# Performance work log

Hardware: AMD Instinct MI355X
Metric: run time of the kernel (lower is better)

## Reference

```python
import jax, jax.numpy as jnp
import numpy as np
from jax import lax

N, T, F_IN = 2048, 32, 5      # stocks, lookback, OHLCV features
H, L, R = 64, 2, 8            # lstm hidden, lstm layers, relation types
GAT_H = 16                    # GAT3 hard-coded hidden width
EDGE_P = 0.05                 # relation-mask edge density
NEG = -1e9


def setup_inputs() -> dict:
    key = jax.random.key(0)
    ks = jax.random.split(key, 20)
    f32 = jnp.float32

    def nrm(k, shape, s=0.1):
        return jax.random.normal(k, shape, f32) * s

    inp = {}
    inp["inputs"] = jax.random.normal(ks[0], (N, T, F_IN), f32)
    inp["relation"] = jax.random.normal(ks[1], (N, N, R), f32)
    mask = jax.random.uniform(ks[2], (N, N)) < EDGE_P
    inp["rel_mask"] = jnp.where(mask, 0.0, NEG).astype(f32)
    # rel_weight: Linear(R, 1)
    inp["rel_w_W"] = nrm(ks[3], (1, R))
    inp["rel_w_b"] = jnp.zeros((1,), f32)
    # 2-layer LSTM (PyTorch layout: w_ih [4H, in], w_hh [4H, H], gate order i,f,g,o)
    inp["w_ih0"] = nrm(ks[4], (4 * H, F_IN)); inp["w_hh0"] = nrm(ks[5], (4 * H, H))
    inp["b_ih0"] = jnp.zeros((4 * H,), f32);  inp["b_hh0"] = jnp.zeros((4 * H,), f32)
    inp["w_ih1"] = nrm(ks[6], (4 * H, H));    inp["w_hh1"] = nrm(ks[7], (4 * H, H))
    inp["b_ih1"] = jnp.zeros((4 * H,), f32);  inp["b_hh1"] = jnp.zeros((4 * H,), f32)
    # GATConv1: hidden -> 16, heads=1 ; GATConv2: 16 -> hidden, heads=1 (lin has no bias in PyG)
    inp["gat1_W"]  = nrm(ks[8], (H, GAT_H));  inp["gat1_as"] = nrm(ks[9], (GAT_H,))
    inp["gat1_ad"] = nrm(ks[10], (GAT_H,));   inp["gat1_b"]  = jnp.zeros((GAT_H,), f32)
    inp["gat2_W"]  = nrm(ks[11], (GAT_H, H)); inp["gat2_as"] = nrm(ks[12], (H,))
    inp["gat2_ad"] = nrm(ks[13], (H,));       inp["gat2_b"]  = jnp.zeros((H,), f32)
    # fc: hidden -> 1
    inp["fc_W"] = nrm(ks[14], (H, 1)); inp["fc_b"] = jnp.zeros((1,), f32)
    return inp


def _lstm_layer(x, w_ih, w_hh, b_ih, b_hh):
    # x: [N, T, in] -> [N, T, H]; PyTorch LSTM equations, zero initial state.
    n = x.shape[0]
    h0 = jnp.zeros((n, w_hh.shape[1]), x.dtype)

    def step(carry, xt):
        h, c = carry
        g = xt @ w_ih.T + h @ w_hh.T + (b_ih + b_hh)   # [N, 4H]
        i, f, gg, o = jnp.split(g, 4, axis=-1)
        c = jax.nn.sigmoid(f) * c + jax.nn.sigmoid(i) * jnp.tanh(gg)
        h = jax.nn.sigmoid(o) * jnp.tanh(c)
        return (h, c), h

    _, hs = lax.scan(step, (h0, h0), jnp.swapaxes(x, 0, 1))  # scan over T
    return jnp.swapaxes(hs, 0, 1)


def _gat(h_in, adj, W, a_s, a_d, b):
    # Dense single-head GATConv over a boolean adjacency adj[src, dst].
    h = h_in @ W                                    # [N, out]
    e = jax.nn.leaky_relu((h @ a_s)[:, None] + (h @ a_d)[None, :], 0.2)  # [src, dst]
    e = jnp.where(adj, e, NEG)
    alpha = jax.nn.softmax(e, axis=0)               # softmax over sources per target
    return alpha.T @ h + b                          # aggregate into targets


def _forward(inputs, relation, rel_mask, rel_w_W, rel_w_b,
             w_ih0, w_hh0, b_ih0, b_hh0, w_ih1, w_hh1, b_ih1, b_hh1,
             gat1_W, gat1_as, gat1_ad, gat1_b,
             gat2_W, gat2_as, gat2_ad, gat2_b, fc_W, fc_b):
    x = _lstm_layer(inputs, w_ih0, w_hh0, b_ih0, b_hh0)
    x = _lstm_layer(x, w_ih1, w_hh1, b_ih1, b_hh1)
    x = x[:, -1, :]                                       # [N, H] last timestep
    rel_w = jnp.einsum('nmr,r->nm', relation, rel_w_W[0]) + rel_w_b[0]  # Linear(R,1)[...,-1]
    inner = x @ x.T                                       # [N, N] similarity
    weight = inner @ rel_w                                # [N, N]
    ws = jax.nn.softmax(rel_mask + weight, axis=1)        # masked entries underflow to 0
    adj = ws > 0                                          # == nonzero edge extraction
    idx = jnp.arange(adj.shape[0])
    adj = adj.at[idx, idx].set(True)                      # GATConv add_self_loops
    h = jax.nn.relu(_gat(x, adj, gat1_W, gat1_as, gat1_ad, gat1_b))
    out = _gat(h, adj, gat2_W, gat2_as, gat2_ad, gat2_b)
    return jax.nn.leaky_relu(out @ fc_W + fc_b, 0.2)      # [N, 1] prediction


def reference(inputs, relation, rel_mask, rel_w_W, rel_w_b,
              w_ih0, w_hh0, b_ih0, b_hh0, w_ih1, w_hh1, b_ih1, b_hh1,
              gat1_W, gat1_as, gat1_ad, gat1_b,
              gat2_W, gat2_as, gat2_ad, gat2_b, fc_W, fc_b):
    return _forward(inputs, relation, rel_mask, rel_w_W, rel_w_b,
                    w_ih0, w_hh0, b_ih0, b_hh0, w_ih1, w_hh1, b_ih1, b_hh1,
                    gat1_W, gat1_as, gat1_ad, gat1_b,
                    gat2_W, gat2_as, gat2_ad, gat2_b, fc_W, fc_b)
```

## Files before the change

### kernel.cpp

```cpp
#include <hip/hip_runtime.h>
#include <math.h>

#define NN 2048
#define TT 32
#define FIN 5
#define HH 64
#define G4 256
#define GATH 16
#define CAP 256

__device__ __forceinline__ float sigf(float x) {
    return 1.0f / (1.0f + __expf(-x));
}
__device__ __forceinline__ float tanh_fast(float x) {
    x = fminf(fmaxf(x, -15.0f), 15.0f);
    float t = __expf(2.0f * x);
    return (t - 1.0f) / (t + 1.0f);
}
__device__ __forceinline__ float dot4(float4 a, float4 b) {
    return a.x * b.x + a.y * b.y + a.z * b.z + a.w * b.w;
}
__device__ __forceinline__ float lrelu_exp(float x) {
    x = (x > 0.0f) ? x : 0.2f * x;
    return __expf(x);
}

#define LNB 2
__global__ __launch_bounds__(256, 1)
void k_lstm(
    const float* __restrict__ inputs,
    const float* __restrict__ w_ih0, const float* __restrict__ w_hh0,
    const float* __restrict__ b_ih0, const float* __restrict__ b_hh0,
    const float* __restrict__ w_ih1, const float* __restrict__ w_hh1,
    const float* __restrict__ b_ih1, const float* __restrict__ b_hh1,
    float* __restrict__ x_out)
{
    __shared__ float x_lds[LNB * TT * FIN];
    __shared__ float hist[LNB][TT + 1][HH];
    __shared__ float g_lds[LNB * G4];
    __shared__ float h1_lds[LNB * HH];

    const int tid = threadIdx.x;
    const int n0 = blockIdx.x * LNB;
    const int g = tid;
    const int cnb = tid >> 6;
    const int ck = tid & 63;

    for (int idx = tid; idx < LNB * TT * FIN; idx += 256)
        x_lds[idx] = inputs[n0 * (TT * FIN) + idx];
    if (tid < LNB * HH) {
        hist[tid >> 6][0][tid & 63] = 0.0f;
        h1_lds[tid] = 0.0f;
    }

    {
        float4 w0[16];
        {
            const float4* p = (const float4*)(w_hh0 + g * HH);
            #pragma unroll
            for (int k = 0; k < 16; ++k) w0[k] = p[k];
        }
        float xw0 = w_ih0[g * FIN + 0];
        float xw1 = w_ih0[g * FIN + 1];
        float xw2 = w_ih0[g * FIN + 2];
        float xw3 = w_ih0[g * FIN + 3];
        float xw4 = w_ih0[g * FIN + 4];
        const float bias0 = b_ih0[g] + b_hh0[g];
        float cA = 0.0f;

        __syncthreads();

        for (int t = 1; t <= TT; ++t) {
            #pragma unroll
            for (int nb = 0; nb < LNB; ++nb) {
                const float4* hv = (const float4*)&hist[nb][t - 1][0];
                float s0 = 0.f, s1 = 0.f, s2 = 0.f, s3 = 0.f;
                #pragma unroll
                for (int k = 0; k < 4; ++k) {
                    s0 += dot4(w0[k],      hv[k]);
                    s1 += dot4(w0[4 + k],  hv[4 + k]);
                    s2 += dot4(w0[8 + k],  hv[8 + k]);
                    s3 += dot4(w0[12 + k], hv[12 + k]);
                }
                const float* xv = &x_lds[nb * (TT * FIN) + (t - 1) * FIN];
                float a = bias0 + xw0 * xv[0] + xw1 * xv[1] + xw2 * xv[2] +
                          xw3 * xv[3] + xw4 * xv[4];
                g_lds[nb * G4 + g] = a + (s0 + s1) + (s2 + s3);
            }
            __syncthreads();
            if (tid < LNB * HH) {
                const int base = cnb * G4 + ck;
                float gi = g_lds[base];
                float gf = g_lds[base + 64];
                float gg = g_lds[base + 128];
                float go = g_lds[base + 192];
                cA = sigf(gf) * cA + sigf(gi) * tanh_fast(gg);
                hist[cnb][t][ck] = sigf(go) * tanh_fast(cA);
            }
            __syncthreads();
        }
    }

    {
        float4 wi[16], wh[16];
        {
            const float4* pi = (const float4*)(w_ih1 + g * HH);
            const float4* ph = (const float4*)(w_hh1 + g * HH);
            #pragma unroll
            for (int k = 0; k < 16; ++k) { wi[k] = pi[k]; wh[k] = ph[k]; }
        }
        const float bias1 = b_ih1[g] + b_hh1[g];
        float cA = 0.0f;

        for (int t = 1; t <= TT; ++t) {
            #pragma unroll
            for (int nb = 0; nb < LNB; ++nb) {
                const float4* xv = (const float4*)&hist[nb][t][0];
                const float4* hv = (const float4*)&h1_lds[nb * HH];
                float s0 = 0.f, s1 = 0.f, s2 = 0.f, s3 = 0.f;
                float u0 = 0.f, u1 = 0.f, u2 = 0.f, u3 = 0.f;
                #pragma unroll
                for (int k = 0; k < 4; ++k) {
                    s0 += dot4(wi[k],      xv[k]);
                    s1 += dot4(wi[4 + k],  xv[4 + k]);
                    s2 += dot4(wi[8 + k],  xv[8 + k]);
                    s3 += dot4(wi[12 + k], xv[12 + k]);
                    u0 += dot4(wh[k],      hv[k]);
                    u1 += dot4(wh[4 + k],  hv[4 + k]);
                    u2 += dot4(wh[8 + k],  hv[8 + k]);
                    u3 += dot4(wh[12 + k], hv[12 + k]);
                }
                g_lds[nb * G4 + g] =
                    bias1 + ((s0 + s1) + (s2 + s3)) + ((u0 + u1) + (u2 + u3));
            }
            __syncthreads();
            if (tid < LNB * HH) {
                const int base = cnb * G4 + ck;
                float gi = g_lds[base];
                float gf = g_lds[base + 64];
                float gg = g_lds[base + 128];
                float go = g_lds[base + 192];
                cA = sigf(gf) * cA + sigf(gi) * tanh_fast(gg);
                float hA = sigf(go) * tanh_fast(cA);
                h1_lds[cnb * HH + ck] = hA;
                if (t == TT) x_out[(n0 + cnb) * HH + ck] = hA;
            }
            __syncthreads();
        }
    }
}

__global__ void k_zero(int* __restrict__ cnt, int* __restrict__ nfull)
{
    int i = blockIdx.x * 256 + threadIdx.x;
    if (i < NN) cnt[i] = 0;
    if (i == 0) *nfull = 0;
}

__global__ __launch_bounds__(256) void k_edges(
    const float* __restrict__ rel_mask,
    int* __restrict__ cnt, int* __restrict__ csc,
    int* __restrict__ row_full, int* __restrict__ full_list,
    int* __restrict__ nfull)
{
    const int i = blockIdx.x;
    const int tid = threadIdx.x;
    __shared__ int s_any;
    if (tid == 0) s_any = 0;
    __syncthreads();
    bool mine = false;
    for (int j = tid; j < NN; j += 256) {
        float rm = rel_mask[i * NN + j];
        bool edge = (rm == 0.0f);
        mine |= edge;
        if (edge && j != i) {
            int slot = atomicAdd(&cnt[j], 1);
            if (slot < CAP) csc[j * CAP + slot] = i;
        }
    }
    if (mine) atomicOr(&s_any, 1);
    __syncthreads();
    if (tid == 0) {
        row_full[i] = s_any ? 0 : 1;
        if (!s_any) {
            int k = atomicAdd(nfull, 1);
            full_list[k] = i;
        }
    }
}

__global__ __launch_bounds__(256) void k_h1(
    const float* __restrict__ x, const float* __restrict__ W,
    const float* __restrict__ a_s, const float* __restrict__ a_d,
    float* __restrict__ h1g, float* __restrict__ es1, float* __restrict__ ed1)
{
    __shared__ float Wl[HH * GATH];
    __shared__ float xl[16 * 65];
    __shared__ float h1l[16 * GATH];
    const int tid = threadIdx.x;
    const int n0 = blockIdx.x * 16;
    for (int idx = tid; idx < HH * GATH; idx += 256) Wl[idx] = W[idx];
    for (int idx = tid; idx < 16 * HH; idx += 256) {
        int ln = idx >> 6, k = idx & 63;
        xl[ln * 65 + k] = x[(n0 + ln) * HH + k];
    }
    __syncthreads();
    const int ln = tid >> 4, jj = tid & 15;
    float acc = 0.0f;
    #pragma unroll 8
    for (int k = 0; k < HH; ++k) acc += xl[ln * 65 + k] * Wl[k * GATH + jj];
    h1g[(n0 + ln) * GATH + jj] = acc;
    h1l[ln * GATH + jj] = acc;
    __syncthreads();
    if (tid < 16) {
        float e_s = 0.0f, e_d = 0.0f;
        #pragma unroll
        for (int t = 0; t < GATH; ++t) {
            float hv = h1l[tid * GATH + t];
            e_s += hv * a_s[t];
            e_d += hv * a_d[t];
        }
        es1[n0 + tid] = e_s;
        ed1[n0 + tid] = e_d;
    }
}

__global__ __launch_bounds__(256) void k_gat1s(
    const int* __restrict__ cnt, const int* __restrict__ csc,
    const int* __restrict__ row_full, const int* __restrict__ full_list,
    const int* __restrict__ nfull,
    const float* __restrict__ h1g, const float* __restrict__ es1,
    const float* __restrict__ ed1, const float* __restrict__ gat1_b,
    float* __restrict__ hrel)
{
    const int tid = threadIdx.x;
    const int lc = tid >> 6;
    const int grp = (tid >> 4) & 3;
    const int d = tid & 15;
    const int j = blockIdx.x * 4 + lc;
    const float edj = ed1[j];
    float acc = 0.0f, l = 0.0f;

    const int n = min(cnt[j], CAP);
    const int* lst = csc + j * CAP;
    for (int e = grp; e < n; e += 4) {
        int i = lst[e];
        float p = lrelu_exp(es1[i] + edj);
        l += p;
        acc += p * h1g[i * GATH + d];
    }
    if (grp == 0 && !row_full[j]) {
        float p = lrelu_exp(es1[j] + edj);
        l += p;
        acc += p * h1g[j * GATH + d];
    }
    const int nf = *nfull;
    for (int f = grp; f < nf; f += 4) {
        int i = full_list[f];
        float p = lrelu_exp(es1[i] + edj);
        l += p;
        acc += p * h1g[i * GATH + d];
    }

    __shared__ float sacc[4][4][GATH];
    __shared__ float sl[4][4];
    sacc[lc][grp][d] = acc;
    if (d == 0) sl[lc][grp] = l;
    __syncthreads();
    if (grp == 0) {
        float a = sacc[lc][0][d] + sacc[lc][1][d] + sacc[lc][2][d] + sacc[lc][3][d];
        float L = sl[lc][0] + sl[lc][1] + sl[lc][2] + sl[lc][3];
        hrel[j * GATH + d] = fmaxf(a / L + gat1_b[d], 0.0f);
    }
}

__global__ __launch_bounds__(256) void k_h2(
    const float* __restrict__ hrel, const float* __restrict__ W2,
    const float* __restrict__ a_s, const float* __restrict__ a_d,
    float* __restrict__ h2g, float* __restrict__ es2, float* __restrict__ ed2)
{
    __shared__ float Wl[GATH * HH];
    __shared__ float hl[4 * 17];
    __shared__ float h2l[4 * HH];
    const int tid = threadIdx.x;
    const int n0 = blockIdx.x * 4;
    for (int idx = tid; idx < GATH * HH; idx += 256) Wl[idx] = W2[idx];
    if (tid < 64) {
        int ln = tid >> 4, k = tid & 15;
        hl[ln * 17 + k] = hrel[(n0 + ln) * GATH + k];
    }
    __syncthreads();
    const int ln = tid >> 6, jj = tid & 63;
    float acc = 0.0f;
    #pragma unroll
    for (int k = 0; k < GATH; ++k) acc += hl[ln * 17 + k] * Wl[k * HH + jj];
    h2g[(n0 + ln) * HH + jj] = acc;
    h2l[ln * HH + jj] = acc;
    __syncthreads();
    if (tid < 4) {
        float e_s = 0.0f, e_d = 0.0f;
        #pragma unroll 16
        for (int t = 0; t < HH; ++t) {
            float hv = h2l[tid * HH + t];
            e_s += hv * a_s[t];
            e_d += hv * a_d[t];
        }
        es2[n0 + tid] = e_s;
        ed2[n0 + tid] = e_d;
    }
}

__global__ __launch_bounds__(256) void k_gat2s(
    const int* __restrict__ cnt, const int* __restrict__ csc,
    const int* __restrict__ row_full, const int* __restrict__ full_list,
    const int* __restrict__ nfull,
    const float* __restrict__ h2g, const float* __restrict__ es2,
    const float* __restrict__ ed2, const float* __restrict__ gat2_b,
    const float* __restrict__ fc_W, const float* __restrict__ fc_b,
    float* __restrict__ out)
{
    const int tid = threadIdx.x;
    const int grp = tid >> 6;
    const int d = tid & 63;
    const int j = blockIdx.x;
    const float edj = ed2[j];
    float acc = 0.0f, l = 0.0f;

    const int n = min(cnt[j], CAP);
    const int* lst = csc + j * CAP;
    for (int e = grp; e < n; e += 4) {
        int i = lst[e];
        float p = lrelu_exp(es2[i] + edj);
        l += p;
        acc += p * h2g[i * HH + d];
    }
    if (grp == 0 && !row_full[j]) {
        float p = lrelu_exp(es2[j] + edj);
        l += p;
        acc += p * h2g[j * HH + d];
    }
    const int nf = *nfull;
    for (int f = grp; f < nf; f += 4) {
        int i = full_list[f];
        float p = lrelu_exp(es2[i] + edj);
        l += p;
        acc += p * h2g[i * HH + d];
    }

    __shared__ float sacc[4][HH];
    __shared__ float sl[4];
    sacc[grp][d] = acc;
    if (d == 0) sl[grp] = l;
    __syncthreads();
    if (grp == 0) {
        float a = sacc[0][d] + sacc[1][d] + sacc[2][d] + sacc[3][d];
        float L = sl[0] + sl[1] + sl[2] + sl[3];
        float v = a / L + gat2_b[d];
        float t = v * fc_W[d];
        #pragma unroll
        for (int off = 32; off >= 1; off >>= 1)
            t += __shfl_down(t, off, 64);
        if (d == 0) {
            float r = t + fc_b[0];
            out[j] = (r > 0.0f) ? r : 0.2f * r;
        }
    }
}

extern "C" void kernel_launch(void* const* d_in, const int* in_sizes, int n_in,
                              void* d_out, int out_size, void* d_ws, size_t ws_size,
                              hipStream_t stream)
{
    const float* inputs   = (const float*)d_in[0];
    const float* rel_mask = (const float*)d_in[2];
    const float* w_ih0 = (const float*)d_in[5];
    const float* w_hh0 = (const float*)d_in[6];
    const float* b_ih0 = (const float*)d_in[7];
    const float* b_hh0 = (const float*)d_in[8];
    const float* w_ih1 = (const float*)d_in[9];
    const float* w_hh1 = (const float*)d_in[10];
    const float* b_ih1 = (const float*)d_in[11];
    const float* b_hh1 = (const float*)d_in[12];
    const float* gat1_W  = (const float*)d_in[13];
    const float* gat1_as = (const float*)d_in[14];
    const float* gat1_ad = (const float*)d_in[15];
    const float* gat1_b  = (const float*)d_in[16];
    const float* gat2_W  = (const float*)d_in[17];
    const float* gat2_as = (const float*)d_in[18];
    const float* gat2_ad = (const float*)d_in[19];
    const float* gat2_b  = (const float*)d_in[20];
    const float* fc_W = (const float*)d_in[21];
    const float* fc_b = (const float*)d_in[22];
    float* out = (float*)d_out;

    float* ws = (float*)d_ws;
    float* x_out = ws;
    float* h1g = x_out + NN * HH;
    float* es1 = h1g + NN * GATH;
    float* ed1 = es1 + NN;
    float* hrel = ed1 + NN;
    float* h2g = hrel + NN * GATH;
    float* es2 = h2g + NN * HH;
    float* ed2 = es2 + NN;
    int* cnt = (int*)(ed2 + NN);
    int* row_full = cnt + NN;
    int* full_list = row_full + NN;
    int* nfull = full_list + NN;
    int* csc = nfull + 8;

    k_zero<<<(NN + 255) / 256, 256, 0, stream>>>(cnt, nfull);
    k_edges<<<NN, 256, 0, stream>>>(rel_mask, cnt, csc, row_full, full_list, nfull);
    k_lstm<<<NN / LNB, 256, 0, stream>>>(inputs, w_ih0, w_hh0, b_ih0, b_hh0,
                                         w_ih1, w_hh1, b_ih1, b_hh1, x_out);
    k_h1<<<NN / 16, 256, 0, stream>>>(x_out, gat1_W, gat1_as, gat1_ad, h1g, es1, ed1);
    k_gat1s<<<NN / 4, 256, 0, stream>>>(cnt, csc, row_full, full_list, nfull,
                                        h1g, es1, ed1, gat1_b, hrel);
    k_h2<<<NN / 4, 256, 0, stream>>>(hrel, gat2_W, gat2_as, gat2_ad, h2g, es2, ed2);
    k_gat2s<<<NN, 256, 0, stream>>>(cnt, csc, row_full, full_list, nfull,
                                    h2g, es2, ed2, gat2_b, fc_W, fc_b, out);
}
```

Before: 491.0 us.

## Split LSTM gate dot-products across lanes and combine gates with wave shuffles

The LSTM kernel now runs 512 threads per block. Each row's dot product is split across two lanes: a half-K split in layer 0, and an input-versus-hidden split in layer 1. The four gates of a cell are then gathered with xor shuffles inside 8 lanes, so each time step needs one barrier instead of two and there is no gate scratch array in LDS. Layer 1 double-buffers its hidden state so the next step can read while the current one writes. The change adds shuffle and select overhead and redundant activation math in 8 lanes per cell, in exchange for less per-thread serial work, fewer barriers and a higher occupancy target in the launch bounds.

```diff
diff --git a/kernel.cpp b/kernel.cpp
--- a/kernel.cpp
+++ b/kernel.cpp
@@ -25,8 +25,19 @@
     return __expf(x);
 }
 
+__device__ __forceinline__ float lstm_combine(float v, float x2, float x4,
+                                              float x6, int gate, float& c)
+{
+    float gi = (gate == 0) ? v  : (gate == 1) ? x2 : (gate == 2) ? x4 : x6;
+    float gf = (gate == 0) ? x2 : (gate == 1) ? v  : (gate == 2) ? x6 : x4;
+    float gg = (gate == 0) ? x4 : (gate == 1) ? x6 : (gate == 2) ? v  : x2;
+    float go = (gate == 0) ? x6 : (gate == 1) ? x4 : (gate == 2) ? x2 : v;
+    c = sigf(gf) * c + sigf(gi) * tanh_fast(gg);
+    return sigf(go) * tanh_fast(c);
+}
+
 #define LNB 2
-__global__ __launch_bounds__(256, 1)
+__global__ __launch_bounds__(512, 4)
 void k_lstm(
     const float* __restrict__ inputs,
     const float* __restrict__ w_ih0, const float* __restrict__ w_hh0,
@@ -35,115 +46,118 @@
     const float* __restrict__ b_ih1, const float* __restrict__ b_hh1,
     float* __restrict__ x_out)
 {
-    __shared__ float x_lds[LNB * TT * FIN];
+    __shared__ float x_lds[LNB][TT * FIN];
     __shared__ float hist[LNB][TT + 1][HH];
-    __shared__ float g_lds[LNB * G4];
-    __shared__ float h1_lds[LNB * HH];
-
-    const int tid = threadIdx.x;
-    const int n0 = blockIdx.x * LNB;
-    const int g = tid;
-    const int cnb = tid >> 6;
-    const int ck = tid & 63;
-
-    for (int idx = tid; idx < LNB * TT * FIN; idx += 256)
-        x_lds[idx] = inputs[n0 * (TT * FIN) + idx];
+    __shared__ float h1buf[2][LNB][HH];
+
+    const int tid  = threadIdx.x;
+    const int kh   = tid & 1;
+    const int gate = (tid >> 1) & 3;
+    const int cell = tid >> 3;
+    const int row  = gate * HH + cell;
+    const int n0   = blockIdx.x * LNB;
+
+    for (int idx = tid; idx < LNB * TT * FIN; idx += 512)
+        ((float*)x_lds)[idx] = inputs[n0 * (TT * FIN) + idx];
     if (tid < LNB * HH) {
         hist[tid >> 6][0][tid & 63] = 0.0f;
-        h1_lds[tid] = 0.0f;
+        h1buf[0][tid >> 6][tid & 63] = 0.0f;
     }
 
     {
-        float4 w0[16];
+        float4 wA[8];
         {
-            const float4* p = (const float4*)(w_hh0 + g * HH);
-            #pragma unroll
-            for (int k = 0; k < 16; ++k) w0[k] = p[k];
-        }
-        float xw0 = w_ih0[g * FIN + 0];
-        float xw1 = w_ih0[g * FIN + 1];
-        float xw2 = w_ih0[g * FIN + 2];
-        float xw3 = w_ih0[g * FIN + 3];
-        float xw4 = w_ih0[g * FIN + 4];
-        const float bias0 = b_ih0[g] + b_hh0[g];
-        float cA = 0.0f;
+            const float4* p = (const float4*)(w_hh0 + row * HH + kh * 32);
+            #pragma unroll
+            for (int k = 0; k < 8; ++k) wA[k] = p[k];
+        }
+        float xw0 = 0.f, xw1 = 0.f, xw2 = 0.f, xw3 = 0.f, xw4 = 0.f;
+        float biasA = 0.f;
+        if (kh == 0) {
+            xw0 = w_ih0[row * FIN + 0];
+            xw1 = w_ih0[row * FIN + 1];
+            xw2 = w_ih0[row * FIN + 2];
+            xw3 = w_ih0[row * FIN + 3];
+            xw4 = w_ih0[row * FIN + 4];
+            biasA = b_ih0[row] + b_hh0[row];
+        }
+        float c0[LNB] = {0.0f, 0.0f};
 
         __syncthreads();
 
         for (int t = 1; t <= TT; ++t) {
+            float vA[LNB];
             #pragma unroll
             for (int nb = 0; nb < LNB; ++nb) {
-                const float4* hv = (const float4*)&hist[nb][t - 1][0];
+                const float4* hv = (const float4*)&hist[nb][t - 1][kh * 32];
+                float s0 = 0.f, s1 = 0.f, s2 = 0.f, s3 = 0.f;
+                #pragma unroll
+                for (int k = 0; k < 2; ++k) {
+                    s0 += dot4(wA[k],     hv[k]);
+                    s1 += dot4(wA[2 + k], hv[2 + k]);
+                    s2 += dot4(wA[4 + k], hv[4 + k]);
+                    s3 += dot4(wA[6 + k], hv[6 + k]);
+                }
+                float s = (s0 + s1) + (s2 + s3);
+                if (kh == 0) {
+                    const float* xv = &x_lds[nb][(t - 1) * FIN];
+                    s += biasA + xw0 * xv[0] + xw1 * xv[1] + xw2 * xv[2] +
+                         xw3 * xv[3] + xw4 * xv[4];
+                }
+                vA[nb] = s;
+            }
+            #pragma unroll
+            for (int nb = 0; nb < LNB; ++nb) {
+                float v = vA[nb] + __shfl_xor(vA[nb], 1);
+                float x2 = __shfl_xor(v, 2);
+                float x4 = __shfl_xor(v, 4);
+                float x6 = __shfl_xor(v, 6);
+                float h = lstm_combine(v, x2, x4, x6, gate, c0[nb]);
+                if ((tid & 7) == 0) hist[nb][t][cell] = h;
+            }
+            __syncthreads();
+        }
+    }
+
+    {
+        float4 wB[16];
+        {
+            const float* wsrc = kh ? w_hh1 : w_ih1;
+            const float4* p = (const float4*)(wsrc + row * HH);
+            #pragma unroll
+            for (int k = 0; k < 16; ++k) wB[k] = p[k];
+        }
+        const float biasB = kh ? 0.0f : (b_ih1[row] + b_hh1[row]);
+        float c1[LNB] = {0.0f, 0.0f};
+
+        for (int t = 1; t <= TT; ++t) {
+            float vB[LNB];
+            #pragma unroll
+            for (int nb = 0; nb < LNB; ++nb) {
+                const float4* av = kh
+                    ? (const float4*)&h1buf[(t - 1) & 1][nb][0]
+                    : (const float4*)&hist[nb][t][0];
                 float s0 = 0.f, s1 = 0.f, s2 = 0.f, s3 = 0.f;
                 #pragma unroll
                 for (int k = 0; k < 4; ++k) {
-                    s0 += dot4(w0[k],      hv[k]);
-                    s1 += dot4(w0[4 + k],  hv[4 + k]);
-                    s2 += dot4(w0[8 + k],  hv[8 + k]);
-                    s3 += dot4(w0[12 + k], hv[12 + k]);
+                    s0 += dot4(wB[k],      av[k]);
+                    s1 += dot4(wB[4 + k],  av[4 + k]);
+                    s2 += dot4(wB[8 + k],  av[8 + k]);
+                    s3 += dot4(wB[12 + k], av[12 + k]);
                 }
-                const float* xv = &x_lds[nb * (TT * FIN) + (t - 1) * FIN];
-                float a = bias0 + xw0 * xv[0] + xw1 * xv[1] + xw2 * xv[2] +
-                          xw3 * xv[3] + xw4 * xv[4];
-                g_lds[nb * G4 + g] = a + (s0 + s1) + (s2 + s3);
+                vB[nb] = biasB + (s0 + s1) + (s2 + s3);
             }
-            __syncthreads();
-            if (tid < LNB * HH) {
-                const int base = cnb * G4 + ck;
-                float gi = g_lds[base];
-                float gf = g_lds[base + 64];
-                float gg = g_lds[base + 128];
-                float go = g_lds[base + 192];
-                cA = sigf(gf) * cA + sigf(gi) * tanh_fast(gg);
-                hist[cnb][t][ck] = sigf(go) * tanh_fast(cA);
-            }
-            __syncthreads();
-        }
-    }
-
-    {
-        float4 wi[16], wh[16];
-        {
-            const float4* pi = (const float4*)(w_ih1 + g * HH);
-            const float4* ph = (const float4*)(w_hh1 + g * HH);
-            #pragma unroll
-            for (int k = 0; k < 16; ++k) { wi[k] = pi[k]; wh[k] = ph[k]; }
-        }
-        const float bias1 = b_ih1[g] + b_hh1[g];
-        float cA = 0.0f;
-
-        for (int t = 1; t <= TT; ++t) {
             #pragma unroll
             for (int nb = 0; nb < LNB; ++nb) {
-                const float4* xv = (const float4*)&hist[nb][t][0];
-                const float4* hv = (const float4*)&h1_lds[nb * HH];
-                float s0 = 0.f, s1 = 0.f, s2 = 0.f, s3 = 0.f;
-                float u0 = 0.f, u1 = 0.f, u2 = 0.f, u3 = 0.f;
-                #pragma unroll
-                for (int k = 0; k < 4; ++k) {
-                    s0 += dot4(wi[k],      xv[k]);
-                    s1 += dot4(wi[4 + k],  xv[4 + k]);
-                    s2 += dot4(wi[8 + k],  xv[8 + k]);
-                    s3 += dot4(wi[12 + k], xv[12 + k]);
-                    u0 += dot4(wh[k],      hv[k]);
-                    u1 += dot4(wh[4 + k],  hv[4 + k]);
-                    u2 += dot4(wh[8 + k],  hv[8 + k]);
-                    u3 += dot4(wh[12 + k], hv[12 + k]);
+                float v = vB[nb] + __shfl_xor(vB[nb], 1);
+                float x2 = __shfl_xor(v, 2);
+                float x4 = __shfl_xor(v, 4);
+                float x6 = __shfl_xor(v, 6);
+                float h = lstm_combine(v, x2, x4, x6, gate, c1[nb]);
+                if ((tid & 7) == 0) {
+                    h1buf[t & 1][nb][cell] = h;
+                    if (t == TT) x_out[(n0 + nb) * HH + cell] = h;
                 }
-                g_lds[nb * G4 + g] =
-                    bias1 + ((s0 + s1) + (s2 + s3)) + ((u0 + u1) + (u2 + u3));
-            }
-            __syncthreads();
-            if (tid < LNB * HH) {
-                const int base = cnb * G4 + ck;
-                float gi = g_lds[base];
-                float gf = g_lds[base + 64];
-                float gg = g_lds[base + 128];
-                float go = g_lds[base + 192];
-                cA = sigf(gf) * cA + sigf(gi) * tanh_fast(gg);
-                float hA = sigf(go) * tanh_fast(cA);
-                h1_lds[cnb * HH + ck] = hA;
-                if (t == TT) x_out[(n0 + cnb) * HH + ck] = hA;
             }
             __syncthreads();
         }
@@ -410,7 +424,7 @@
 
     k_zero<<<(NN + 255) / 256, 256, 0, stream>>>(cnt, nfull);
     k_edges<<<NN, 256, 0, stream>>>(rel_mask, cnt, csc, row_full, full_list, nfull);
-    k_lstm<<<NN / LNB, 256, 0, stream>>>(inputs, w_ih0, w_hh0, b_ih0, b_hh0,
+    k_lstm<<<NN / LNB, 512, 0, stream>>>(inputs, w_ih0, w_hh0, b_ih0, b_hh0,
                                          w_ih1, w_hh1, b_ih1, b_hh1, x_out);
     k_h1<<<NN / 16, 256, 0, stream>>>(x_out, gat1_W, gat1_as, gat1_ad, h1g, es1, ed1);
     k_gat1s<<<NN / 4, 256, 0, stream>>>(cnt, csc, row_full, full_list, nfull,
```

After: 757.6 us. +54.3%, slower.

## Co-schedule edge extraction with LSTM blocks and fuse GAT1 aggregation with GAT2 projection

Applied to the files above, without the earlier changes.

The edge-extraction kernel is merged into the LSTM kernel. Odd blocks scan two relation-mask rows each, and even blocks run the LSTM recurrence, so the memory-bound mask scan can overlap the latency-bound LSTM. The GAT layer-1 aggregation kernel now also does the layer-2 linear projection and attention-score computation from shared memory, which removes the k_h2 launch and the hrel round-trip through global memory. In exchange, edge blocks carry the LSTM kernel's launch bounds and shared-memory footprint, and W2 is read from global memory per thread instead of being staged in LDS.

```diff
diff --git a/kernel.cpp b/kernel.cpp
--- a/kernel.cpp
+++ b/kernel.cpp
@@ -25,23 +25,68 @@
     return __expf(x);
 }
 
+__global__ void k_zero(int* __restrict__ cnt, int* __restrict__ nfull)
+{
+    int i = blockIdx.x * 256 + threadIdx.x;
+    if (i < NN) cnt[i] = 0;
+    if (i == 0) *nfull = 0;
+}
+
 #define LNB 2
 __global__ __launch_bounds__(256, 1)
-void k_lstm(
+void k_lstm_edges(
     const float* __restrict__ inputs,
     const float* __restrict__ w_ih0, const float* __restrict__ w_hh0,
     const float* __restrict__ b_ih0, const float* __restrict__ b_hh0,
     const float* __restrict__ w_ih1, const float* __restrict__ w_hh1,
     const float* __restrict__ b_ih1, const float* __restrict__ b_hh1,
-    float* __restrict__ x_out)
-{
+    float* __restrict__ x_out,
+    const float* __restrict__ rel_mask,
+    int* __restrict__ cnt, int* __restrict__ csc,
+    int* __restrict__ row_full, int* __restrict__ full_list,
+    int* __restrict__ nfull)
+{
+    const int tid = threadIdx.x;
+
+    if (blockIdx.x & 1) {
+        __shared__ int s_any[2];
+        const int r0 = (blockIdx.x >> 1) * 2;
+        if (tid < 2) s_any[tid] = 0;
+        __syncthreads();
+        #pragma unroll
+        for (int rr = 0; rr < 2; ++rr) {
+            const int i = r0 + rr;
+            bool mine = false;
+            for (int j = tid; j < NN; j += 256) {
+                float rm = rel_mask[i * NN + j];
+                bool edge = (rm == 0.0f);
+                mine |= edge;
+                if (edge && j != i) {
+                    int slot = atomicAdd(&cnt[j], 1);
+                    if (slot < CAP) csc[j * CAP + slot] = i;
+                }
+            }
+            if (mine) atomicOr(&s_any[rr], 1);
+        }
+        __syncthreads();
+        if (tid < 2) {
+            const int i = r0 + tid;
+            int any = s_any[tid];
+            row_full[i] = any ? 0 : 1;
+            if (!any) {
+                int k = atomicAdd(nfull, 1);
+                full_list[k] = i;
+            }
+        }
+        return;
+    }
+
     __shared__ float x_lds[LNB * TT * FIN];
     __shared__ float hist[LNB][TT + 1][HH];
     __shared__ float g_lds[LNB * G4];
     __shared__ float h1_lds[LNB * HH];
 
-    const int tid = threadIdx.x;
-    const int n0 = blockIdx.x * LNB;
+    const int n0 = (blockIdx.x >> 1) * LNB;
     const int g = tid;
     const int cnb = tid >> 6;
     const int ck = tid & 63;
@@ -150,45 +195,6 @@
     }
 }
 
-__global__ void k_zero(int* __restrict__ cnt, int* __restrict__ nfull)
-{
-    int i = blockIdx.x * 256 + threadIdx.x;
-    if (i < NN) cnt[i] = 0;
-    if (i == 0) *nfull = 0;
-}
-
-__global__ __launch_bounds__(256) void k_edges(
-    const float* __restrict__ rel_mask,
-    int* __restrict__ cnt, int* __restrict__ csc,
-    int* __restrict__ row_full, int* __restrict__ full_list,
-    int* __restrict__ nfull)
-{
-    const int i = blockIdx.x;
-    const int tid = threadIdx.x;
-    __shared__ int s_any;
-    if (tid == 0) s_any = 0;
-    __syncthreads();
-    bool mine = false;
-    for (int j = tid; j < NN; j += 256) {
-        float rm = rel_mask[i * NN + j];
-        bool edge = (rm == 0.0f);
-        mine |= edge;
-        if (edge && j != i) {
-            int slot = atomicAdd(&cnt[j], 1);
-            if (slot < CAP) csc[j * CAP + slot] = i;
-        }
-    }
-    if (mine) atomicOr(&s_any, 1);
-    __syncthreads();
-    if (tid == 0) {
-        row_full[i] = s_any ? 0 : 1;
-        if (!s_any) {
-            int k = atomicAdd(nfull, 1);
-            full_list[k] = i;
-        }
-    }
-}
-
 __global__ __launch_bounds__(256) void k_h1(
     const float* __restrict__ x, const float* __restrict__ W,
     const float* __restrict__ a_s, const float* __restrict__ a_d,
@@ -225,13 +231,15 @@
     }
 }
 
-__global__ __launch_bounds__(256) void k_gat1s(
+__global__ __launch_bounds__(256) void k_gat1s2(
     const int* __restrict__ cnt, const int* __restrict__ csc,
     const int* __restrict__ row_full, const int* __restrict__ full_list,
     const int* __restrict__ nfull,
     const float* __restrict__ h1g, const float* __restrict__ es1,
     const float* __restrict__ ed1, const float* __restrict__ gat1_b,
-    float* __restrict__ hrel)
+    const float* __restrict__ W2,
+    const float* __restrict__ a_s2, const float* __restrict__ a_d2,
+    float* __restrict__ h2g, float* __restrict__ es2, float* __restrict__ ed2)
 {
     const int tid = threadIdx.x;
     const int lc = tid >> 6;
@@ -264,49 +272,39 @@
 
     __shared__ float sacc[4][4][GATH];
     __shared__ float sl[4][4];
+    __shared__ float hl[4][GATH];
+    __shared__ float h2l[4][HH];
     sacc[lc][grp][d] = acc;
     if (d == 0) sl[lc][grp] = l;
     __syncthreads();
     if (grp == 0) {
         float a = sacc[lc][0][d] + sacc[lc][1][d] + sacc[lc][2][d] + sacc[lc][3][d];
         float L = sl[lc][0] + sl[lc][1] + sl[lc][2] + sl[lc][3];
-        hrel[j * GATH + d] = fmaxf(a / L + gat1_b[d], 0.0f);
-    }
-}
-
-__global__ __launch_bounds__(256) void k_h2(
-    const float* __restrict__ hrel, const float* __restrict__ W2,
-    const float* __restrict__ a_s, const float* __restrict__ a_d,
-    float* __restrict__ h2g, float* __restrict__ es2, float* __restrict__ ed2)
-{
-    __shared__ float Wl[GATH * HH];
-    __shared__ float hl[4 * 17];
-    __shared__ float h2l[4 * HH];
-    const int tid = threadIdx.x;
-    const int n0 = blockIdx.x * 4;
-    for (int idx = tid; idx < GATH * HH; idx += 256) Wl[idx] = W2[idx];
-    if (tid < 64) {
-        int ln = tid >> 4, k = tid & 15;
-        hl[ln * 17 + k] = hrel[(n0 + ln) * GATH + k];
-    }
-    __syncthreads();
-    const int ln = tid >> 6, jj = tid & 63;
-    float acc = 0.0f;
-    #pragma unroll
-    for (int k = 0; k < GATH; ++k) acc += hl[ln * 17 + k] * Wl[k * HH + jj];
-    h2g[(n0 + ln) * HH + jj] = acc;
-    h2l[ln * HH + jj] = acc;
+        hl[lc][d] = fmaxf(a / L + gat1_b[d], 0.0f);
+    }
+    __syncthreads();
+    {
+        const int lc2 = tid >> 6;
+        const int jj = tid & 63;
+        float acc2 = 0.0f;
+        #pragma unroll
+        for (int k = 0; k < GATH; ++k)
+            acc2 += hl[lc2][k] * W2[k * HH + jj];
+        const int j2 = blockIdx.x * 4 + lc2;
+        h2g[j2 * HH + jj] = acc2;
+        h2l[lc2][jj] = acc2;
+    }
     __syncthreads();
     if (tid < 4) {
         float e_s = 0.0f, e_d = 0.0f;
         #pragma unroll 16
         for (int t = 0; t < HH; ++t) {
-            float hv = h2l[tid * HH + t];
-            e_s += hv * a_s[t];
-            e_d += hv * a_d[t];
-        }
-        es2[n0 + tid] = e_s;
-        ed2[n0 + tid] = e_d;
+            float hv = h2l[tid][t];
+            e_s += hv * a_s2[t];
+            e_d += hv * a_d2[t];
+        }
+        es2[blockIdx.x * 4 + tid] = e_s;
+        ed2[blockIdx.x * 4 + tid] = e_d;
     }
 }
 
@@ -409,13 +407,15 @@
     int* csc = nfull + 8;
 
     k_zero<<<(NN + 255) / 256, 256, 0, stream>>>(cnt, nfull);
-    k_edges<<<NN, 256, 0, stream>>>(rel_mask, cnt, csc, row_full, full_list, nfull);
-    k_lstm<<<NN / LNB, 256, 0, stream>>>(inputs, w_ih0, w_hh0, b_ih0, b_hh0,
-                                         w_ih1, w_hh1, b_ih1, b_hh1, x_out);
+    k_lstm_edges<<<NN, 256, 0, stream>>>(inputs, w_ih0, w_hh0, b_ih0, b_hh0,
+                                         w_ih1, w_hh1, b_ih1, b_hh1, x_out,
+                                         rel_mask, cnt, csc, row_full,
+                                         full_list, nfull);
     k_h1<<<NN / 16, 256, 0, stream>>>(x_out, gat1_W, gat1_as, gat1_ad, h1g, es1, ed1);
-    k_gat1s<<<NN / 4, 256, 0, stream>>>(cnt, csc, row_full, full_list, nfull,
-                                        h1g, es1, ed1, gat1_b, hrel);
-    k_h2<<<NN / 4, 256, 0, stream>>>(hrel, gat2_W, gat2_as, gat2_ad, h2g, es2, ed2);
+    k_gat1s2<<<NN / 4, 256, 0, stream>>>(cnt, csc, row_full, full_list, nfull,
+                                         h1g, es1, ed1, gat1_b,
+                                         gat2_W, gat2_as, gat2_ad,
+                                         h2g, es2, ed2);
     k_gat2s<<<NN, 256, 0, stream>>>(cnt, csc, row_full, full_list, nfull,
                                     h2g, es2, ed2, gat2_b, fc_W, fc_b, out);
 }
```

New measurement: 599.4 us. +22.1%, slower.
